# Performance work log

Hardware: AMD Instinct MI355X
Metric: run time of the kernel (lower is better)

## Reference

```python
import jax, jax.numpy as jnp
import numpy as np

B, N, C_IN, C_OUT, R_IN, R_OUT, NUM_PSI, E = 4, 1024, 128, 256, 32, 32, 2, 65536


def psi(x, src, dst, W, b):
    # GIN-style GNN layer: aggregate neighbors via scatter-add, then linear+relu
    agg = jax.ops.segment_sum(x[src], dst, num_segments=x.shape[0])
    return jax.nn.relu((x + agg) @ W + b)


def setup_inputs() -> dict:
    key = jax.random.key(0)
    ks = jax.random.split(key, 12)
    inp = {
        'x_s': jax.random.normal(ks[0], (B * N, C_IN), jnp.float32),
        'edge_index_s': jax.random.randint(ks[1], (2, E), 0, B * N, jnp.int32),
        'x_t': jax.random.normal(ks[2], (B * N, C_IN), jnp.float32),
        'edge_index_t': jax.random.randint(ks[3], (2, E), 0, B * N, jnp.int32),
        'r': jax.random.normal(ks[4], (NUM_PSI, B, N, R_IN), jnp.float32),
        'W1': jax.random.normal(ks[5], (C_IN, C_OUT), jnp.float32) * (0.2 / np.sqrt(C_IN)),
        'b1': jnp.zeros((C_OUT,), jnp.float32),
        'Wp': jax.random.normal(ks[6], (NUM_PSI, R_IN, R_OUT), jnp.float32) * (1.0 / np.sqrt(R_IN)),
        'bp': jnp.zeros((NUM_PSI, R_OUT), jnp.float32),
        'Wm1': jax.random.normal(ks[7], (R_OUT, R_OUT), jnp.float32) * (1.0 / np.sqrt(R_OUT)),
        'bm1': jnp.zeros((R_OUT,), jnp.float32),
        'Wm2': jax.random.normal(ks[8], (R_OUT, 1), jnp.float32) * (1.0 / np.sqrt(R_OUT)),
        'bm2': jnp.zeros((1,), jnp.float32),
        'sum_weights': jnp.ones((NUM_PSI + 1,), jnp.float32),
    }
    return inp


def reference(x_s, edge_index_s, x_t, edge_index_t, r, W1, b1, Wp, bp, Wm1, bm1, Wm2, bm2, sum_weights):
    src_s, dst_s = edge_index_s[0], edge_index_s[1]
    src_t, dst_t = edge_index_t[0], edge_index_t[1]
    # psi_1 node embeddings, then dense-batch (equal-size graphs -> masks all true)
    h_s = psi(x_s, src_s, dst_s, W1, b1).reshape(B, N, C_OUT)
    h_t = psi(x_t, src_t, dst_t, W1, b1).reshape(B, N, C_OUT)
    S_hat = jnp.einsum('bsc,btc->bst', h_s, h_t)  # [B, N_s, N_t]
    S_0 = jax.nn.softmax(S_hat, axis=-1)
    S_stack = []
    for i in range(NUM_PSI):  # structurally distinct psi modules
        S = jax.nn.softmax(S_hat, axis=-1)
        r_s = r[i]  # [B, N, R_IN] random node indicators
        r_t = jnp.einsum('bst,bsr->btr', S, r_s)
        o_s = psi(r_s.reshape(B * N, R_IN), src_s, dst_s, Wp[i], bp[i]).reshape(B, N, R_OUT)
        o_t = psi(r_t.reshape(B * N, R_IN), src_t, dst_t, Wp[i], bp[i]).reshape(B, N, R_OUT)
        D = o_s[:, :, None, :] - o_t[:, None, :, :]  # [B, N_s, N_t, R_OUT]
        upd = (jax.nn.relu(D @ Wm1 + bm1) @ Wm2 + bm2)[..., 0]
        S_hat = S_hat + upd
        S_stack.append(jax.nn.softmax(S_hat, axis=-1))
    S_final = sum_weights[0] * S_0
    for i in range(NUM_PSI):
        S_final = S_final + sum_weights[i + 1] * S_stack[i]
    return jax.nn.softmax(S_final.reshape(B * N, N), axis=-1)
```

## Files before the change

### kernel.cpp

```cpp
#include <hip/hip_runtime.h>
#include <hip/hip_bf16.h>

#define NBATCH 4
#define NSEQ   1024
#define BNN    4096
#define CIN    128
#define COUT   256
#define RDIM   32
#define NEDGE  65536

__global__ void edge_hist(const int* __restrict__ ei_s, const int* __restrict__ ei_t,
                          int* __restrict__ cnt) {
    int gid = blockIdx.x * blockDim.x + threadIdx.x;
    int list = gid >> 16;
    int e = gid & (NEDGE - 1);
    const int* ei = list ? ei_t : ei_s;
    atomicAdd(&cnt[list * BNN + ei[NEDGE + e]], 1);
}

__global__ void edge_scan(const int* __restrict__ cnt, int* __restrict__ offs,
                          int* __restrict__ cursor) {
    __shared__ int sums[256];
    int list = blockIdx.x;
    int tid = threadIdx.x;
    int local[16];
    int s = 0;
#pragma unroll
    for (int k = 0; k < 16; k++) { local[k] = cnt[list * BNN + tid * 16 + k]; s += local[k]; }
    sums[tid] = s;
    __syncthreads();
    for (int off = 1; off < 256; off <<= 1) {
        int v = 0;
        if (tid >= off) v = sums[tid - off];
        __syncthreads();
        if (tid >= off) sums[tid] += v;
        __syncthreads();
    }
    int run = tid ? sums[tid - 1] : 0;
#pragma unroll
    for (int k = 0; k < 16; k++) {
        offs[list * (BNN + 1) + tid * 16 + k] = run;
        cursor[list * BNN + tid * 16 + k] = run;
        run += local[k];
    }
    if (tid == 255) offs[list * (BNN + 1) + BNN] = run;
}

__global__ void edge_place(const int* __restrict__ ei_s, const int* __restrict__ ei_t,
                           int* __restrict__ cursor, int* __restrict__ ssrc) {
    int gid = blockIdx.x * blockDim.x + threadIdx.x;
    int list = gid >> 16;
    int e = gid & (NEDGE - 1);
    const int* ei = list ? ei_t : ei_s;
    int dst = ei[NEDGE + e], src = ei[e];
    int p = atomicAdd(&cursor[list * BNN + dst], 1);
    ssrc[list * NEDGE + p] = src;
}

__global__ void gather_agg128(const float* __restrict__ x_s, const float* __restrict__ x_t,
                              const int* __restrict__ offs, const int* __restrict__ ssrc,
                              float* __restrict__ t_s, float* __restrict__ t_t) {
    __shared__ int sl[128];
    int node = blockIdx.x & (BNN - 1);
    int list = blockIdx.x >> 12;
    const float* x = list ? x_t : x_s;
    float* t = list ? t_t : t_s;
    int c = threadIdx.x;
    int beg = offs[list * (BNN + 1) + node], end = offs[list * (BNN + 1) + node + 1];
    float acc = x[(size_t)node * CIN + c];
    for (int base = beg; base < end; base += 128) {
        int cnt = min(128, end - base);
        __syncthreads();
        if (c < cnt) sl[c] = ssrc[list * NEDGE + base + c];
        __syncthreads();
        int e = 0;
        for (; e + 4 <= cnt; e += 4) {
            int n0 = sl[e], n1 = sl[e + 1], n2 = sl[e + 2], n3 = sl[e + 3];
            acc += x[(size_t)n0 * CIN + c] + x[(size_t)n1 * CIN + c]
                 + x[(size_t)n2 * CIN + c] + x[(size_t)n3 * CIN + c];
        }
        for (; e < cnt; e++) acc += x[(size_t)sl[e] * CIN + c];
    }
    t[(size_t)node * CIN + c] = acc;
}

__global__ void gather_agg32(const float* __restrict__ rs, const float* __restrict__ rtin,
                             const int* __restrict__ offs, const int* __restrict__ ssrc,
                             float* __restrict__ trs, float* __restrict__ trt) {
    int list = blockIdx.y;
    int node = blockIdx.x * 8 + (threadIdx.x >> 5);
    int c = threadIdx.x & 31;
    const float* in = list ? rtin : rs;
    float* outp = list ? trt : trs;
    int beg = offs[list * (BNN + 1) + node], end = offs[list * (BNN + 1) + node + 1];
    float acc = in[(size_t)node * RDIM + c];
    for (int e = beg; e < end; e++)
        acc += in[(size_t)ssrc[list * NEDGE + e] * RDIM + c];
    outp[(size_t)node * RDIM + c] = acc;
}

__global__ void psi1_gemm(const float* __restrict__ t_s, const float* __restrict__ t_t,
                          const float* __restrict__ W1, const float* __restrict__ b1,
                          float* __restrict__ h_s, float* __restrict__ h_t) {
    __shared__ float rows[8][CIN];
    int half = blockIdx.x >> 9;
    const float* t = half ? t_t : t_s;
    float* h = half ? h_t : h_s;
    int r0 = (blockIdx.x & 511) * 8;
    int tid = threadIdx.x;
    {
        int rr = tid >> 5, c4 = (tid & 31) << 2;
        *(float4*)&rows[rr][c4] = *(const float4*)(t + (size_t)(r0 + rr) * CIN + c4);
    }
    __syncthreads();
    float acc[8];
    float bias = b1[tid];
#pragma unroll
    for (int r = 0; r < 8; r++) acc[r] = bias;
    for (int k = 0; k < CIN; k++) {
        float w = W1[k * COUT + tid];
#pragma unroll
        for (int r = 0; r < 8; r++) acc[r] = fmaf(rows[r][k], w, acc[r]);
    }
#pragma unroll
    for (int r = 0; r < 8; r++)
        h[(size_t)(r0 + r) * COUT + tid] = fmaxf(acc[r], 0.f);
}

__global__ __launch_bounds__(256) void shat_gemm(const float* __restrict__ hs,
                                                 const float* __restrict__ ht,
                                                 float* __restrict__ Sh) {
    __shared__ float As[16][68];
    __shared__ float Bs[16][68];
    int flat = blockIdx.x;
    int swz = (flat & 7) * 128 + (flat >> 3);
    int bx = swz & 15, by = (swz >> 4) & 15, bz = swz >> 8;
    int b  = bz;
    int s0 = by * 64, t0 = bx * 64;
    const float* A  = hs + (size_t)b * NSEQ * COUT;
    const float* Bm = ht + (size_t)b * NSEQ * COUT;
    int tid = threadIdx.x;
    int tx = tid & 15, ty = tid >> 4;
    int lr = tid >> 2, lk = (tid & 3) << 2;
    const float* Ap = A  + (size_t)(s0 + lr) * COUT + lk;
    const float* Bp = Bm + (size_t)(t0 + lr) * COUT + lk;
    float4 a0 = *(const float4*)(Ap);
    float4 b0 = *(const float4*)(Bp);
    float acc[4][4] = {};
    for (int kp = 0; kp < 16; kp++) {
        __syncthreads();
        As[lk + 0][lr] = a0.x; As[lk + 1][lr] = a0.y;
        As[lk + 2][lr] = a0.z; As[lk + 3][lr] = a0.w;
        Bs[lk + 0][lr] = b0.x; Bs[lk + 1][lr] = b0.y;
        Bs[lk + 2][lr] = b0.z; Bs[lk + 3][lr] = b0.w;
        __syncthreads();
        if (kp < 15) {
            a0 = *(const float4*)(Ap + (kp + 1) * 16);
            b0 = *(const float4*)(Bp + (kp + 1) * 16);
        }
#pragma unroll
        for (int k = 0; k < 16; k++) {
            float av[4], bv[4];
            *(float4*)&av[0] = *(const float4*)&As[k][ty * 4];
            *(float4*)&bv[0] = *(const float4*)&Bs[k][tx * 4];
#pragma unroll
            for (int i = 0; i < 4; i++)
#pragma unroll
                for (int j = 0; j < 4; j++)
                    acc[i][j] = fmaf(av[i], bv[j], acc[i][j]);
        }
    }
#pragma unroll
    for (int i = 0; i < 4; i++) {
        float4 v = make_float4(acc[i][0], acc[i][1], acc[i][2], acc[i][3]);
        *(float4*)(Sh + ((size_t)b * NSEQ + s0 + ty * 4 + i) * NSEQ + t0 + tx * 4) = v;
    }
}

__global__ void softmax_stats(const float* __restrict__ Sh, float* __restrict__ mstat,
                              float* __restrict__ istat) {
    int row = blockIdx.x, tid = threadIdx.x;
    float4 v = *(const float4*)(Sh + (size_t)row * NSEQ + tid * 4);
    float m = fmaxf(fmaxf(v.x, v.y), fmaxf(v.z, v.w));
#pragma unroll
    for (int o = 32; o; o >>= 1) m = fmaxf(m, __shfl_xor(m, o));
    __shared__ float redm[4], reds[4];
    int wid = tid >> 6, lane = tid & 63;
    if (lane == 0) redm[wid] = m;
    __syncthreads();
    m = fmaxf(fmaxf(redm[0], redm[1]), fmaxf(redm[2], redm[3]));
    float s = __expf(v.x - m) + __expf(v.y - m) + __expf(v.z - m) + __expf(v.w - m);
#pragma unroll
    for (int o = 32; o; o >>= 1) s += __shfl_xor(s, o);
    if (lane == 0) reds[wid] = s;
    __syncthreads();
    if (tid == 0) {
        float tot = reds[0] + reds[1] + reds[2] + reds[3];
        mstat[row] = m;
        istat[row] = 1.0f / tot;
    }
}

__global__ void softmax_final3(const float* __restrict__ Sh0, const float* __restrict__ Sh1,
                               const float* __restrict__ Sh2, const float* __restrict__ m0a,
                               const float* __restrict__ i0a, const float* __restrict__ m1a,
                               const float* __restrict__ i1a, const float* __restrict__ sw,
                               float* __restrict__ out) {
    int row = blockIdx.x, tid = threadIdx.x;
    __shared__ float red[4];
    int wid = tid >> 6, lane = tid & 63;
    float4 v0 = *(const float4*)(Sh0 + (size_t)row * NSEQ + tid * 4);
    float4 v1 = *(const float4*)(Sh1 + (size_t)row * NSEQ + tid * 4);
    float4 v2 = *(const float4*)(Sh2 + (size_t)row * NSEQ + tid * 4);
    float m2 = fmaxf(fmaxf(v2.x, v2.y), fmaxf(v2.z, v2.w));
#pragma unroll
    for (int o = 32; o; o >>= 1) m2 = fmaxf(m2, __shfl_xor(m2, o));
    if (lane == 0) red[wid] = m2;
    __syncthreads();
    m2 = fmaxf(fmaxf(red[0], red[1]), fmaxf(red[2], red[3]));
    __syncthreads();
    float4 e2;
    e2.x = __expf(v2.x - m2); e2.y = __expf(v2.y - m2);
    e2.z = __expf(v2.z - m2); e2.w = __expf(v2.w - m2);
    float s2 = e2.x + e2.y + e2.z + e2.w;
#pragma unroll
    for (int o = 32; o; o >>= 1) s2 += __shfl_xor(s2, o);
    if (lane == 0) red[wid] = s2;
    __syncthreads();
    s2 = red[0] + red[1] + red[2] + red[3];
    __syncthreads();
    float w0 = sw[0] * i0a[row], w1 = sw[1] * i1a[row], w2 = sw[2] / s2;
    float m0 = m0a[row], m1 = m1a[row];
    float4 f;
    f.x = fmaf(w0, __expf(v0.x - m0), fmaf(w1, __expf(v1.x - m1), w2 * e2.x));
    f.y = fmaf(w0, __expf(v0.y - m0), fmaf(w1, __expf(v1.y - m1), w2 * e2.y));
    f.z = fmaf(w0, __expf(v0.z - m0), fmaf(w1, __expf(v1.z - m1), w2 * e2.z));
    f.w = fmaf(w0, __expf(v0.w - m0), fmaf(w1, __expf(v1.w - m1), w2 * e2.w));
    float mf = fmaxf(fmaxf(f.x, f.y), fmaxf(f.z, f.w));
#pragma unroll
    for (int o = 32; o; o >>= 1) mf = fmaxf(mf, __shfl_xor(mf, o));
    if (lane == 0) red[wid] = mf;
    __syncthreads();
    mf = fmaxf(fmaxf(red[0], red[1]), fmaxf(red[2], red[3]));
    __syncthreads();
    float4 ef;
    ef.x = __expf(f.x - mf); ef.y = __expf(f.y - mf);
    ef.z = __expf(f.z - mf); ef.w = __expf(f.w - mf);
    float sf = ef.x + ef.y + ef.z + ef.w;
#pragma unroll
    for (int o = 32; o; o >>= 1) sf += __shfl_xor(sf, o);
    if (lane == 0) red[wid] = sf;
    __syncthreads();
    sf = red[0] + red[1] + red[2] + red[3];
    float inv = 1.0f / sf;
    float4 sv = make_float4(ef.x * inv, ef.y * inv, ef.z * inv, ef.w * inv);
    *(float4*)(out + (size_t)row * NSEQ + tid * 4) = sv;
}

__global__ void rt_part(const float* __restrict__ Sh, const float* __restrict__ mstat,
                        const float* __restrict__ istat, const float* __restrict__ rs,
                        float* __restrict__ part) {
    __shared__ float rsld[64][33];
    __shared__ float ml[64], il[64];
    int b = blockIdx.z, t0 = blockIdx.y * 128, s0 = blockIdx.x * 64;
    int tid = threadIdx.x;
    if (tid < 64) ml[tid] = mstat[b * NSEQ + s0 + tid];
    else if (tid < 128) il[tid - 64] = istat[b * NSEQ + s0 + tid - 64];
#pragma unroll
    for (int q = 0; q < 2; q++) {
        int lid = (tid << 1) + q;
        int srow = lid >> 3, c4 = (lid & 7) << 2;
        float4 v = *(const float4*)(rs + ((size_t)b * NSEQ + s0 + srow) * RDIM + c4);
        rsld[srow][c4] = v.x; rsld[srow][c4 + 1] = v.y;
        rsld[srow][c4 + 2] = v.z; rsld[srow][c4 + 3] = v.w;
    }
    __syncthreads();
    int t = t0 + (tid & 127);
    int j0 = (tid >> 7) << 4;
    float acc[16] = {};
    const float* Sp = Sh + ((size_t)b * NSEQ + s0) * NSEQ + t;
#pragma unroll 8
    for (int s = 0; s < 64; s++) {
        float p = __expf(Sp[(size_t)s * NSEQ] - ml[s]) * il[s];
#pragma unroll
        for (int j = 0; j < 16; j++) acc[j] = fmaf(p, rsld[s][j0 + j], acc[j]);
    }
    float* pp = part + (((size_t)blockIdx.x * NBATCH + b) * NSEQ + t) * RDIM + j0;
#pragma unroll
    for (int j4 = 0; j4 < 16; j4 += 4)
        *(float4*)(pp + j4) = make_float4(acc[j4], acc[j4 + 1], acc[j4 + 2], acc[j4 + 3]);
}

__global__ void rt_reduce(const float* __restrict__ part, float* __restrict__ rt) {
    int i = blockIdx.x * blockDim.x + threadIdx.x;
    const float4* p = (const float4*)part + i;
    float4 a = make_float4(0.f, 0.f, 0.f, 0.f);
#pragma unroll
    for (int c = 0; c < 16; c++) {
        float4 v = p[(size_t)c * (BNN * RDIM / 4)];
        a.x += v.x; a.y += v.y; a.z += v.z; a.w += v.w;
    }
    ((float4*)rt)[i] = a;
}

__global__ void psi_r(const float* __restrict__ trs, const float* __restrict__ trt,
                      const float* __restrict__ Wp, const float* __restrict__ bp,
                      const float* __restrict__ Wm1, const float* __restrict__ bm1,
                      float* __restrict__ Ps, float* __restrict__ Pt) {
    __shared__ float sWp[32 * 32], sWm1[32 * 32];
    __shared__ float srow[8][33], so[8][33];
    int which = blockIdx.y;
    const float* t_r = which ? trt : trs;
    float* P = which ? Pt : Ps;
    int tid = threadIdx.x;
#pragma unroll
    for (int q = 0; q < 4; q++) {
        sWp[tid + q * 256]  = Wp[tid + q * 256];
        sWm1[tid + q * 256] = Wm1[tid + q * 256];
    }
    int g = tid >> 5, j = tid & 31;
    int row = blockIdx.x * 8 + g;
    srow[g][j] = t_r[(size_t)row * RDIM + j];
    __syncthreads();
    float acc = bp[j];
#pragma unroll
    for (int k = 0; k < 32; k++) acc = fmaf(srow[g][k], sWp[k * 32 + j], acc);
    float o = fmaxf(acc, 0.f);
    so[g][j] = o;
    __syncthreads();
    float acc2 = which ? 0.f : bm1[j];
#pragma unroll
    for (int k = 0; k < 32; k++) acc2 = fmaf(so[g][k], sWm1[k * 32 + j], acc2);
    P[(size_t)row * RDIM + j] = acc2;
}

__global__ __launch_bounds__(256) void upd_add(const float* __restrict__ Ps,
                                               const float* __restrict__ Pt,
                                               const float* __restrict__ Wm2,
                                               const float* __restrict__ bm2p,
                                               const float* __restrict__ Shin,
                                               float* __restrict__ Shout) {
    __shared__ float sPs[128][33], sPt[64][33];
    __shared__ float swm[32];
    int b = blockIdx.z, s0 = blockIdx.y * 128, t0 = blockIdx.x * 64;
    int tid = threadIdx.x;
#pragma unroll
    for (int q = 0; q < 4; q++) {
        int lid = (tid << 2) + q, rr = lid >> 3, c4 = (lid & 7) << 2;
        float4 a = *(const float4*)(Ps + ((size_t)b * NSEQ + s0 + rr) * RDIM + c4);
        sPs[rr][c4] = a.x; sPs[rr][c4 + 1] = a.y; sPs[rr][c4 + 2] = a.z; sPs[rr][c4 + 3] = a.w;
    }
#pragma unroll
    for (int q = 0; q < 2; q++) {
        int lid = (tid << 1) + q, rr = lid >> 3, c4 = (lid & 7) << 2;
        float4 c = *(const float4*)(Pt + ((size_t)b * NSEQ + t0 + rr) * RDIM + c4);
        sPt[rr][c4] = c.x; sPt[rr][c4 + 1] = c.y; sPt[rr][c4 + 2] = c.z; sPt[rr][c4 + 3] = c.w;
    }
    if (tid < 32) swm[tid] = Wm2[tid];
    __syncthreads();
    float bm2 = bm2p[0];
    int tx = tid & 15, ty = tid >> 4;
    float acc[8][4] = {};
#pragma unroll
    for (int k = 0; k < 32; k++) {
        float w = swm[k];
        float ps[8], pt[4];
#pragma unroll
        for (int i = 0; i < 8; i++) ps[i] = sPs[ty * 8 + i][k];
#pragma unroll
        for (int j = 0; j < 4; j++) pt[j] = sPt[tx * 4 + j][k];
#pragma unroll
        for (int i = 0; i < 8; i++)
#pragma unroll
            for (int j = 0; j < 4; j++)
                acc[i][j] = fmaf(fmaxf(ps[i] - pt[j], 0.f), w, acc[i][j]);
    }
#pragma unroll
    for (int i = 0; i < 8; i++) {
        size_t base = ((size_t)b * NSEQ + s0 + ty * 8 + i) * NSEQ + t0 + tx * 4;
        float4 old = *(const float4*)(Shin + base);
        old.x += acc[i][0] + bm2; old.y += acc[i][1] + bm2;
        old.z += acc[i][2] + bm2; old.w += acc[i][3] + bm2;
        *(float4*)(Shout + base) = old;
    }
}

extern "C" void kernel_launch(void* const* d_in, const int* in_sizes, int n_in,
                              void* d_out, int out_size, void* d_ws, size_t ws_size,
                              hipStream_t stream) {
    const float* x_s  = (const float*)d_in[0];
    const int*   ei_s = (const int*)  d_in[1];
    const float* x_t  = (const float*)d_in[2];
    const int*   ei_t = (const int*)  d_in[3];
    const float* r    = (const float*)d_in[4];
    const float* W1   = (const float*)d_in[5];
    const float* b1   = (const float*)d_in[6];
    const float* Wp   = (const float*)d_in[7];
    const float* bp   = (const float*)d_in[8];
    const float* Wm1  = (const float*)d_in[9];
    const float* bm1  = (const float*)d_in[10];
    const float* Wm2  = (const float*)d_in[11];
    const float* bm2  = (const float*)d_in[12];
    const float* sw   = (const float*)d_in[13];
    float* out = (float*)d_out;

    float* ws = (float*)d_ws;
    float* t_s  = ws;  ws += (size_t)BNN * CIN;
    float* t_t  = ws;  ws += (size_t)BNN * CIN;
    float* h_s  = ws;  ws += (size_t)BNN * COUT;
    float* h_t  = ws;  ws += (size_t)BNN * COUT;
    float* Sh0  = ws;  ws += (size_t)NBATCH * NSEQ * NSEQ;
    float* Sh1  = ws;  ws += (size_t)NBATCH * NSEQ * NSEQ;
    float* Sh2  = ws;  ws += (size_t)NBATCH * NSEQ * NSEQ;
    float* mstat = ws; ws += 2 * BNN;
    float* istat = ws; ws += 2 * BNN;
    float* rt   = ws;  ws += (size_t)BNN * RDIM;
    float* trs  = ws;  ws += (size_t)BNN * RDIM;
    float* trt  = ws;  ws += (size_t)BNN * RDIM;
    float* Ps   = ws;  ws += (size_t)BNN * RDIM;
    float* Pt   = ws;  ws += (size_t)BNN * RDIM;
    int* icnt  = (int*)ws;
    int* ioffs = icnt  + 2 * BNN;
    int* icur  = ioffs + 2 * (BNN + 1);
    int* issrc = icur  + 2 * BNN;
    float* rtpart = h_s;

    float* ShA[3] = {Sh0, Sh1, Sh2};

    hipMemsetAsync(icnt, 0, 2 * BNN * sizeof(int), stream);
    edge_hist <<<512, 256, 0, stream>>>(ei_s, ei_t, icnt);
    edge_scan <<<2, 256, 0, stream>>>(icnt, ioffs, icur);
    edge_place<<<512, 256, 0, stream>>>(ei_s, ei_t, icur, issrc);

    gather_agg128<<<8192, 128, 0, stream>>>(x_s, x_t, ioffs, issrc, t_s, t_t);
    psi1_gemm<<<1024, 256, 0, stream>>>(t_s, t_t, W1, b1, h_s, h_t);
    shat_gemm<<<1024, 256, 0, stream>>>(h_s, h_t, Sh0);

    for (int i = 0; i < 2; i++) {
        softmax_stats<<<4096, 256, 0, stream>>>(ShA[i], mstat + i * BNN, istat + i * BNN);
        rt_part<<<dim3(16, 8, 4), 256, 0, stream>>>(ShA[i], mstat + i * BNN, istat + i * BNN,
                                                    r + (size_t)i * BNN * RDIM, rtpart);
        rt_reduce<<<128, 256, 0, stream>>>(rtpart, rt);
        gather_agg32<<<dim3(512, 2), 256, 0, stream>>>(r + (size_t)i * BNN * RDIM, rt,
                                                       ioffs, issrc, trs, trt);
        psi_r<<<dim3(512, 2), 256, 0, stream>>>(trs, trt, Wp + i * RDIM * RDIM,
                                                bp + i * RDIM, Wm1, bm1, Ps, Pt);
        upd_add<<<dim3(16, 8, 4), 256, 0, stream>>>(Ps, Pt, Wm2, bm2, ShA[i], ShA[i + 1]);
    }
    softmax_final3<<<4096, 256, 0, stream>>>(Sh0, Sh1, Sh2, mstat, istat,
                                             mstat + BNN, istat + BNN, sw, out);
}
```

Measured before the change: 210.3 us.

## Rewrite relu pair term via abs identity and transpose smem tiles in upd_add

After: 203.7 us. -3.1%, faster.

```diff
diff --git a/kernel.cpp b/kernel.cpp
--- a/kernel.cpp
+++ b/kernel.cpp
@@ -306,18 +306,23 @@
 __global__ void psi_r(const float* __restrict__ trs, const float* __restrict__ trt,
                       const float* __restrict__ Wp, const float* __restrict__ bp,
                       const float* __restrict__ Wm1, const float* __restrict__ bm1,
-                      float* __restrict__ Ps, float* __restrict__ Pt) {
+                      const float* __restrict__ Wm2,
+                      float* __restrict__ Ps, float* __restrict__ Pt,
+                      float* __restrict__ Aps, float* __restrict__ Apt) {
     __shared__ float sWp[32 * 32], sWm1[32 * 32];
     __shared__ float srow[8][33], so[8][33];
+    __shared__ float swm2[32];
     int which = blockIdx.y;
     const float* t_r = which ? trt : trs;
     float* P = which ? Pt : Ps;
+    float* A = which ? Apt : Aps;
     int tid = threadIdx.x;
 #pragma unroll
     for (int q = 0; q < 4; q++) {
         sWp[tid + q * 256]  = Wp[tid + q * 256];
         sWm1[tid + q * 256] = Wm1[tid + q * 256];
     }
+    if (tid < 32) swm2[tid] = Wm2[tid];
     int g = tid >> 5, j = tid & 31;
     int row = blockIdx.x * 8 + g;
     srow[g][j] = t_r[(size_t)row * RDIM + j];
@@ -332,56 +337,71 @@
 #pragma unroll
     for (int k = 0; k < 32; k++) acc2 = fmaf(so[g][k], sWm1[k * 32 + j], acc2);
     P[(size_t)row * RDIM + j] = acc2;
+    float v = acc2 * swm2[j];
+#pragma unroll
+    for (int o2 = 16; o2; o2 >>= 1) v += __shfl_xor(v, o2, 32);
+    if (j == 0) A[row] = v;
 }
 
 __global__ __launch_bounds__(256) void upd_add(const float* __restrict__ Ps,
                                                const float* __restrict__ Pt,
+                                               const float* __restrict__ Aps,
+                                               const float* __restrict__ Apt,
                                                const float* __restrict__ Wm2,
                                                const float* __restrict__ bm2p,
                                                const float* __restrict__ Shin,
                                                float* __restrict__ Shout) {
-    __shared__ float sPs[128][33], sPt[64][33];
+    __shared__ float sPsT[32][68];
+    __shared__ float sPtT[32][68];
     __shared__ float swm[32];
-    int b = blockIdx.z, s0 = blockIdx.y * 128, t0 = blockIdx.x * 64;
-    int tid = threadIdx.x;
-#pragma unroll
-    for (int q = 0; q < 4; q++) {
-        int lid = (tid << 2) + q, rr = lid >> 3, c4 = (lid & 7) << 2;
-        float4 a = *(const float4*)(Ps + ((size_t)b * NSEQ + s0 + rr) * RDIM + c4);
-        sPs[rr][c4] = a.x; sPs[rr][c4 + 1] = a.y; sPs[rr][c4 + 2] = a.z; sPs[rr][c4 + 3] = a.w;
-    }
-#pragma unroll
-    for (int q = 0; q < 2; q++) {
-        int lid = (tid << 1) + q, rr = lid >> 3, c4 = (lid & 7) << 2;
-        float4 c = *(const float4*)(Pt + ((size_t)b * NSEQ + t0 + rr) * RDIM + c4);
-        sPt[rr][c4] = c.x; sPt[rr][c4 + 1] = c.y; sPt[rr][c4 + 2] = c.z; sPt[rr][c4 + 3] = c.w;
+    __shared__ float sAs[64], sAt[64];
+    int b = blockIdx.z, s0 = blockIdx.y * 64, t0 = blockIdx.x * 64;
+    int tid = threadIdx.x;
+    {
+        int lr = tid >> 2, lk = (tid & 3) << 3;
+        const float* p = Ps + ((size_t)b * NSEQ + s0 + lr) * RDIM + lk;
+        float4 v0 = *(const float4*)p, v1 = *(const float4*)(p + 4);
+        sPsT[lk + 0][lr] = v0.x; sPsT[lk + 1][lr] = v0.y;
+        sPsT[lk + 2][lr] = v0.z; sPsT[lk + 3][lr] = v0.w;
+        sPsT[lk + 4][lr] = v1.x; sPsT[lk + 5][lr] = v1.y;
+        sPsT[lk + 6][lr] = v1.z; sPsT[lk + 7][lr] = v1.w;
+        const float* q = Pt + ((size_t)b * NSEQ + t0 + lr) * RDIM + lk;
+        float4 u0 = *(const float4*)q, u1 = *(const float4*)(q + 4);
+        sPtT[lk + 0][lr] = u0.x; sPtT[lk + 1][lr] = u0.y;
+        sPtT[lk + 2][lr] = u0.z; sPtT[lk + 3][lr] = u0.w;
+        sPtT[lk + 4][lr] = u1.x; sPtT[lk + 5][lr] = u1.y;
+        sPtT[lk + 6][lr] = u1.z; sPtT[lk + 7][lr] = u1.w;
     }
     if (tid < 32) swm[tid] = Wm2[tid];
-    __syncthreads();
-    float bm2 = bm2p[0];
+    else if (tid < 96)  sAs[tid - 32] = Aps[b * NSEQ + s0 + tid - 32];
+    else if (tid < 160) sAt[tid - 96] = Apt[b * NSEQ + t0 + tid - 96];
+    __syncthreads();
     int tx = tid & 15, ty = tid >> 4;
-    float acc[8][4] = {};
-#pragma unroll
+    float acc[4][4] = {};
+#pragma unroll 8
     for (int k = 0; k < 32; k++) {
         float w = swm[k];
-        float ps[8], pt[4];
-#pragma unroll
-        for (int i = 0; i < 8; i++) ps[i] = sPs[ty * 8 + i][k];
-#pragma unroll
-        for (int j = 0; j < 4; j++) pt[j] = sPt[tx * 4 + j][k];
-#pragma unroll
-        for (int i = 0; i < 8; i++)
+        float ps[4], pt[4];
+        *(float4*)&ps[0] = *(const float4*)&sPsT[k][ty * 4];
+        *(float4*)&pt[0] = *(const float4*)&sPtT[k][tx * 4];
+#pragma unroll
+        for (int i = 0; i < 4; i++)
 #pragma unroll
             for (int j = 0; j < 4; j++)
-                acc[i][j] = fmaf(fmaxf(ps[i] - pt[j], 0.f), w, acc[i][j]);
-    }
-#pragma unroll
-    for (int i = 0; i < 8; i++) {
-        size_t base = ((size_t)b * NSEQ + s0 + ty * 8 + i) * NSEQ + t0 + tx * 4;
+                acc[i][j] = fmaf(fabsf(ps[i] - pt[j]), w, acc[i][j]);
+    }
+    float bm2 = bm2p[0];
+#pragma unroll
+    for (int i = 0; i < 4; i++) {
+        float as = sAs[ty * 4 + i];
+        size_t base = ((size_t)b * NSEQ + s0 + ty * 4 + i) * NSEQ + t0 + tx * 4;
         float4 old = *(const float4*)(Shin + base);
-        old.x += acc[i][0] + bm2; old.y += acc[i][1] + bm2;
-        old.z += acc[i][2] + bm2; old.w += acc[i][3] + bm2;
-        *(float4*)(Shout + base) = old;
+        float4 f;
+        f.x = old.x + 0.5f * (acc[i][0] + as - sAt[tx * 4 + 0]) + bm2;
+        f.y = old.y + 0.5f * (acc[i][1] + as - sAt[tx * 4 + 1]) + bm2;
+        f.z = old.z + 0.5f * (acc[i][2] + as - sAt[tx * 4 + 2]) + bm2;
+        f.w = old.w + 0.5f * (acc[i][3] + as - sAt[tx * 4 + 3]) + bm2;
+        *(float4*)(Shout + base) = f;
     }
 }
 
@@ -419,6 +439,8 @@
     float* trt  = ws;  ws += (size_t)BNN * RDIM;
     float* Ps   = ws;  ws += (size_t)BNN * RDIM;
     float* Pt   = ws;  ws += (size_t)BNN * RDIM;
+    float* Aps  = ws;  ws += BNN;
+    float* Apt  = ws;  ws += BNN;
     int* icnt  = (int*)ws;
     int* ioffs = icnt  + 2 * BNN;
     int* icur  = ioffs + 2 * (BNN + 1);
@@ -444,8 +466,10 @@
         gather_agg32<<<dim3(512, 2), 256, 0, stream>>>(r + (size_t)i * BNN * RDIM, rt,
                                                        ioffs, issrc, trs, trt);
         psi_r<<<dim3(512, 2), 256, 0, stream>>>(trs, trt, Wp + i * RDIM * RDIM,
-                                                bp + i * RDIM, Wm1, bm1, Ps, Pt);
-        upd_add<<<dim3(16, 8, 4), 256, 0, stream>>>(Ps, Pt, Wm2, bm2, ShA[i], ShA[i + 1]);
+                                                bp + i * RDIM, Wm1, bm1, Wm2,
+                                                Ps, Pt, Aps, Apt);
+        upd_add<<<dim3(16, 16, 4), 256, 0, stream>>>(Ps, Pt, Aps, Apt, Wm2, bm2,
+                                                     ShA[i], ShA[i + 1]);
     }
     softmax_final3<<<4096, 256, 0, stream>>>(Sh0, Sh1, Sh2, mstat, istat,
                                              mstat + BNN, istat + BNN, sw, out);
```
